# Kernel tuning notes

Hardware: AMD Instinct MI355X
Metric: run time of the kernel (lower is better)

Reference implementation:

```python
import jax, jax.numpy as jnp
import numpy as np

N_NODES = 50000
N_EDGES = 200000
HID = 32
EDGE_DIM = 16
EDGE_HIDDEN = 128


def setup_inputs() -> dict:
    key = jax.random.key(0)
    ks = jax.random.split(key, 10)
    nf = jax.random.normal(ks[0], (N_NODES, HID), dtype=jnp.float32)
    ef = jax.random.normal(ks[1], (N_EDGES, EDGE_DIM), dtype=jnp.float32)
    edge_src = jax.random.randint(ks[2], (N_EDGES,), 0, N_NODES, dtype=jnp.int32)
    edge_dst = jax.random.randint(ks[3], (N_EDGES,), 0, N_NODES, dtype=jnp.int32)
    # edge_func MLP: EDGE_DIM -> EDGE_HIDDEN -> HID*HID (per-edge weight matrix)
    s1 = 1.0 / np.sqrt(EDGE_DIM)
    s2 = 1.0 / np.sqrt(EDGE_HIDDEN)
    W1 = jax.random.uniform(ks[4], (EDGE_DIM, EDGE_HIDDEN), jnp.float32, -s1, s1)
    b1 = jax.random.uniform(ks[5], (EDGE_HIDDEN,), jnp.float32, -s1, s1)
    W2 = jax.random.uniform(ks[6], (EDGE_HIDDEN, HID * HID), jnp.float32, -s2, s2)
    b2 = jax.random.uniform(ks[7], (HID * HID,), jnp.float32, -s2, s2)
    bias = jnp.zeros((HID,), dtype=jnp.float32)  # NNConv output bias
    return {"nf": nf, "ef": ef, "edge_src": edge_src, "edge_dst": edge_dst,
            "W1": W1, "b1": b1, "W2": W2, "b2": b2, "bias": bias}


def reference(nf, ef, edge_src, edge_dst, W1, b1, W2, b2, bias):
    # edge network: per-edge weight matrix [E, HID, HID]
    h = jax.nn.relu(ef @ W1 + b1)
    We = (h @ W2 + b2).reshape(-1, HID, HID)
    # gather source features, per-edge matvec message [E, HID]
    msg = jnp.einsum('ei,eio->eo', nf[edge_src], We)
    # sum-aggregate messages at destination nodes, add bias
    agg = jax.ops.segment_sum(msg, edge_dst, num_segments=nf.shape[0])
    return agg + bias
```

## Files before the change

kernel.cpp:

```cpp
#include <hip/hip_runtime.h>


#define E_TOTAL   200000
#define N_NODES   50000
#define TILES     3125
#define OUT4      400000
#define OUT4_BLKS 1563
#define W2C_BLKS  64
#define NBLK      256
#define NTL_BIG   53
#define LDS_BYTES 163840

typedef short short8  __attribute__((ext_vector_type(8)));
typedef float f32x4   __attribute__((ext_vector_type(4)));
typedef float f32x16  __attribute__((ext_vector_type(16)));

__device__ __forceinline__ short f2bf(float f) {
    union { float f; unsigned u; } cv; cv.f = f;
    unsigned r = cv.u + 0x7fffu + ((cv.u >> 16) & 1u);
    return (short)(r >> 16);
}

__device__ __forceinline__ void gll16(const short* gsrc, short* ldst) {
    __builtin_amdgcn_global_load_lds(
        (const __attribute__((address_space(1))) unsigned int*)gsrc,
        (__attribute__((address_space(3))) unsigned int*)ldst, 16, 0, 0);
}

__global__ __launch_bounds__(256) void setup_kernel(const float* __restrict__ W2,
                                                    const float* __restrict__ bias,
                                                    float* __restrict__ out,
                                                    short* __restrict__ W2p) {
    int bid = blockIdx.x, tid = threadIdx.x;
    if (bid < OUT4_BLKS) {
        int i4 = bid * 256 + tid;
        if (i4 < OUT4) {
            float4 bv = *(const float4*)(bias + ((i4 & 7) << 2));
            *(float4*)(out + (size_t)i4 * 4) = bv;
        }
    } else {
        int q = (bid - OUT4_BLKS) * 256 + tid;
        int p  = q >> 13;
        int ch = q & 8191;
        int ks = ch >> 10, ct = (ch >> 6) & 15, lhg = (ch >> 5) & 1, cc = ch & 31;
        int c  = ct * 32 + cc;
        int i  = c >> 4, o15 = c & 15;
        int ci = i * 32 + p * 16 + o15;
        int kb = ks * 16 + lhg * 8;
        short8 pk;
        #pragma unroll
        for (int j = 0; j < 8; ++j) pk[j] = f2bf(W2[(size_t)(kb + j) * 1024 + ci]);
        *(short8*)(W2p + (size_t)q * 8) = pk;
    }
}

__global__ __launch_bounds__(512, 2) void mpnn_kernel(const float* __restrict__ nf,
                                                      const float* __restrict__ ef,
                                                      const int*   __restrict__ esrc,
                                                      const int*   __restrict__ edst,
                                                      const float* __restrict__ W1,
                                                      const float* __restrict__ b1,
                                                      const float* __restrict__ b2,
                                                      const short* __restrict__ W2p,
                                                      float* __restrict__ out) {
    extern __shared__ __align__(16) unsigned char smem[];
    short* W2s  = (short*)(smem);
    short* W1Ts = (short*)(smem + 131072);
    short* Hs   = (short*)(smem + 135168);
    float* XsT  = (float*)(smem + 151552);
    float* pbuf = (float*)(smem + 131072);

    const int tid = threadIdx.x;
    const int w   = tid >> 6;
    const int l31 = tid & 31;
    const int lh  = (tid >> 5) & 1;
    const int o15 = l31 & 15;
    const int ib  = l31 >> 4;
    const int xbw = lh ^ ib;
    const int bid = blockIdx.x;
    const int ntl = (bid < NTL_BIG) ? 13 : 12;
    const int itn = 2 * ntl;

    float4 xreg; short8 efreg;
    float  b2v0, b2v1;
    {
        #pragma unroll
        for (int j = 0; j < 16; ++j)
            gll16(W2p + w * 8192 + j * 512 + (tid & 63) * 8, W2s + w * 8192 + j * 512);
    }
    {
        int g = tid * 4; int i = g >> 7; int c0 = g & 127;
        float4 v = *(const float4*)(W1 + g);
        float vv[4] = {v.x, v.y, v.z, v.w};
        #pragma unroll
        for (int u = 0; u < 4; ++u) {
            int c = c0 + u;
            W1Ts[c * 16 + (((i >> 3) ^ ((c >> 2) & 1)) << 3) + (i & 7)] = f2bf(vv[u]);
        }
    }
    {
        int s = esrc[bid * 64 + (tid >> 3)];
        xreg = *(const float4*)(nf + (size_t)s * 32 + (tid & 7) * 4);
        int eL = l31 + ((w & 1) << 5);
        const float* ep = ef + (size_t)(bid * 64 + eL) * 16 + lh * 8;
        float4 a0 = *(const float4*)(ep);
        float4 a1 = *(const float4*)(ep + 4);
        efreg[0] = f2bf(a0.x); efreg[1] = f2bf(a0.y); efreg[2] = f2bf(a0.z); efreg[3] = f2bf(a0.w);
        efreg[4] = f2bf(a1.x); efreg[5] = f2bf(a1.y); efreg[6] = f2bf(a1.z); efreg[7] = f2bf(a1.w);
    }
    b2v0 = b2[(4 * w + ib) * 32 + o15];
    b2v1 = b2[(4 * w + 2 + ib) * 32 + o15];
    const int   cW1  = ((w >> 1) << 5) + l31;
    const float b1v  = b1[cW1];

    __syncthreads();
    const short8 w1frag = *(const short8*)(W1Ts + cW1 * 16 + ((lh ^ ((cW1 >> 2) & 1)) << 3));

    float  pv0 = 0.f, pv1 = 0.f;
    float *pa0 = out, *pa1 = out;

    for (int it = 0; it < itn; ++it) {
        const int pass = (it >= ntl) ? 1 : 0;
        const int tile = bid + (it - pass * ntl) * NBLK;
        const int ebase = tile * 64;

        if (it == ntl) {
            #pragma unroll
            for (int j = 0; j < 16; ++j)
                gll16(W2p + 65536 + w * 8192 + j * 512 + (tid & 63) * 8, W2s + w * 8192 + j * 512);
            b2v0 = b2[(4 * w + ib) * 32 + 16 + o15];
            b2v1 = b2[(4 * w + 2 + ib) * 32 + 16 + o15];
        }
        __syncthreads();

        {
            int e = tid >> 3, i4 = (tid & 7) * 4;
            XsT[(i4 + 0) * 68 + e] = xreg.x;
            XsT[(i4 + 1) * 68 + e] = xreg.y;
            XsT[(i4 + 2) * 68 + e] = xreg.z;
            XsT[(i4 + 3) * 68 + e] = xreg.w;
        }

        {
            f32x16 hacc;
            #pragma unroll
            for (int q = 0; q < 16; ++q) hacc[q] = 0.f;
            hacc = __builtin_amdgcn_mfma_f32_32x32x16_bf16(efreg, w1frag, hacc, 0, 0, 0);
            const int mh = w & 1, G1 = cW1 >> 3, j1 = cW1 & 7;
            #pragma unroll
            for (int r = 0; r < 16; ++r) {
                int ee = (r & 3) + ((r >> 2) << 3) + (lh << 2) + (mh << 5);
                float v = fmaxf(hacc[r] + b1v, 0.f);
                Hs[G1 * 512 + ((ee ^ (G1 & 7)) << 3) + j1] = f2bf(v);
            }
        }
        __syncthreads();

        int nit = it + 1; if (nit >= itn) nit = it;
        const int npass = (nit >= ntl) ? 1 : 0;
        const int nebase = (bid + (nit - npass * ntl) * NBLK) * 64;

        f32x16 acc00, acc01, acc10, acc11;
        #pragma unroll
        for (int q = 0; q < 16; ++q) { acc00[q] = 0.f; acc01[q] = 0.f; acc10[q] = 0.f; acc11[q] = 0.f; }
        int pre_s = 0;
        #pragma unroll
        for (int ks = 0; ks < 8; ++ks) {
            const int G  = 2 * ks + lh;
            const int ax = ((l31 ^ (G & 7)) << 3);
            short8 afr0 = *(const short8*)(Hs + G * 512 + ax);
            short8 afr1 = *(const short8*)(Hs + G * 512 + ax + 256);
            short8 bfr0 = *(const short8*)(W2s + ks * 8192 + (2 * w    ) * 512 + lh * 256 + l31 * 8);
            short8 bfr1 = *(const short8*)(W2s + ks * 8192 + (2 * w + 1) * 512 + lh * 256 + l31 * 8);
            acc00 = __builtin_amdgcn_mfma_f32_32x32x16_bf16(afr0, bfr0, acc00, 0, 0, 0);
            acc01 = __builtin_amdgcn_mfma_f32_32x32x16_bf16(afr1, bfr0, acc01, 0, 0, 0);
            acc10 = __builtin_amdgcn_mfma_f32_32x32x16_bf16(afr0, bfr1, acc10, 0, 0, 0);
            acc11 = __builtin_amdgcn_mfma_f32_32x32x16_bf16(afr1, bfr1, acc11, 0, 0, 0);
            if (ks == 1) pre_s = esrc[nebase + (tid >> 3)];
            if (ks == 2 && it > 0) {
                atomicAdd(pa0, pv0);
                atomicAdd(pa1, pv1);
            }
            if (ks == 3) {
                int eL = l31 + ((w & 1) << 5);
                const float* ep = ef + (size_t)(nebase + eL) * 16 + lh * 8;
                float4 a0 = *(const float4*)(ep);
                float4 a1 = *(const float4*)(ep + 4);
                efreg[0] = f2bf(a0.x); efreg[1] = f2bf(a0.y); efreg[2] = f2bf(a0.z); efreg[3] = f2bf(a0.w);
                efreg[4] = f2bf(a1.x); efreg[5] = f2bf(a1.y); efreg[6] = f2bf(a1.z); efreg[7] = f2bf(a1.w);
            }
            if (ks == 5) xreg = *(const float4*)(nf + (size_t)pre_s * 32 + (tid & 7) * 4);
        }

        const int xc0 = 4 * w + ib, xc1 = 4 * w + 2 + ib;
        float sv0[16], sv1[16];
        #pragma unroll
        for (int rq = 0; rq < 4; ++rq) {
            const int eb = 8 * rq + 4 * lh;
            f32x4 A0 = *(const f32x4*)(XsT + xc0 * 68 + eb);
            f32x4 B0 = *(const f32x4*)(XsT + xc1 * 68 + eb);
            f32x4 A1 = *(const f32x4*)(XsT + xc0 * 68 + eb + 32);
            f32x4 B1 = *(const f32x4*)(XsT + xc1 * 68 + eb + 32);
            #pragma unroll
            for (int u = 0; u < 4; ++u) {
                int r = rq * 4 + u;
                float v = A0[u] * (acc00[r] + b2v0) + B0[u] * (acc10[r] + b2v1);
                v += __shfl_xor(v, 16);
                sv0[r] = v;
                float v1 = A1[u] * (acc01[r] + b2v0) + B1[u] * (acc11[r] + b2v1);
                v1 += __shfl_xor(v1, 16);
                sv1[r] = v1;
            }
        }

        __syncthreads();
        #pragma unroll
        for (int r = 0; r < 16; ++r) {
            int e = (r & 3) + ((r >> 2) << 3) + (lh << 2) + (ib << 5);
            pbuf[(w << 10) + ((e ^ xbw) << 4) + o15] = ib ? sv1[r] : sv0[r];
        }
        __syncthreads();
        {
            int idx = tid;
            int e = idx >> 4, oo = idx & 15;
            int xbE = ((e >> 2) ^ (e >> 5)) & 1;
            int a = ((e ^ xbE) << 4) + oo;
            pv0 = ((pbuf[a]          + pbuf[a + 1024]) + (pbuf[a + 2048] + pbuf[a + 3072]))
                + ((pbuf[a + 4096]   + pbuf[a + 5120]) + (pbuf[a + 6144] + pbuf[a + 7168]));
            pa0 = out + (size_t)edst[ebase + e] * 32 + (pass << 4) + oo;
            idx = tid + 512;
            e = idx >> 4; oo = idx & 15;
            xbE = ((e >> 2) ^ (e >> 5)) & 1;
            a = ((e ^ xbE) << 4) + oo;
            pv1 = ((pbuf[a]          + pbuf[a + 1024]) + (pbuf[a + 2048] + pbuf[a + 3072]))
                + ((pbuf[a + 4096]   + pbuf[a + 5120]) + (pbuf[a + 6144] + pbuf[a + 7168]));
            pa1 = out + (size_t)edst[ebase + e] * 32 + (pass << 4) + oo;
        }
    }
    atomicAdd(pa0, pv0);
    atomicAdd(pa1, pv1);
}

extern "C" void kernel_launch(void* const* d_in, const int* in_sizes, int n_in,
                              void* d_out, int out_size, void* d_ws, size_t ws_size,
                              hipStream_t stream) {
    const float* nf   = (const float*)d_in[0];
    const float* ef   = (const float*)d_in[1];
    const int*   src  = (const int*)  d_in[2];
    const int*   dst  = (const int*)  d_in[3];
    const float* W1   = (const float*)d_in[4];
    const float* b1   = (const float*)d_in[5];
    const float* W2   = (const float*)d_in[6];
    const float* b2   = (const float*)d_in[7];
    const float* bias = (const float*)d_in[8];
    float* out = (float*)d_out;
    short* W2p = (short*)d_ws;

    static bool init_done = false;
    if (!init_done) {
        hipFuncSetAttribute((const void*)mpnn_kernel,
                            hipFuncAttributeMaxDynamicSharedMemorySize, LDS_BYTES);
        init_done = true;
    }

    setup_kernel<<<OUT4_BLKS + W2C_BLKS, 256, 0, stream>>>(W2, bias, out, W2p);
    mpnn_kernel<<<NBLK, 512, LDS_BYTES, stream>>>(nf, ef, src, dst, W1, b1, b2, W2p, out);
}
```

Baseline: 167.5 us.

## Stream W2 fragments from global into registers to double block count

```diff
diff --git a/kernel.cpp b/kernel.cpp
--- a/kernel.cpp
+++ b/kernel.cpp
@@ -7,9 +7,9 @@
 #define OUT4      400000
 #define OUT4_BLKS 1563
 #define W2C_BLKS  64
-#define NBLK      256
+#define NBLK      512
 #define NTL_BIG   53
-#define LDS_BYTES 163840
+#define LDS_BYTES 61952
 
 typedef short short8  __attribute__((ext_vector_type(8)));
 typedef float f32x4   __attribute__((ext_vector_type(4)));
@@ -19,12 +19,6 @@
     union { float f; unsigned u; } cv; cv.f = f;
     unsigned r = cv.u + 0x7fffu + ((cv.u >> 16) & 1u);
     return (short)(r >> 16);
-}
-
-__device__ __forceinline__ void gll16(const short* gsrc, short* ldst) {
-    __builtin_amdgcn_global_load_lds(
-        (const __attribute__((address_space(1))) unsigned int*)gsrc,
-        (__attribute__((address_space(3))) unsigned int*)ldst, 16, 0, 0);
 }
 
 __global__ __launch_bounds__(256) void setup_kernel(const float* __restrict__ W2,
@@ -54,7 +48,7 @@
     }
 }
 
-__global__ __launch_bounds__(512, 2) void mpnn_kernel(const float* __restrict__ nf,
+__global__ __launch_bounds__(512, 4) void mpnn_kernel(const float* __restrict__ nf,
                                                       const float* __restrict__ ef,
                                                       const int*   __restrict__ esrc,
                                                       const int*   __restrict__ edst,
@@ -64,11 +58,10 @@
                                                       const short* __restrict__ W2p,
                                                       float* __restrict__ out) {
     extern __shared__ __align__(16) unsigned char smem[];
-    short* W2s  = (short*)(smem);
-    short* W1Ts = (short*)(smem + 131072);
-    short* Hs   = (short*)(smem + 135168);
-    float* XsT  = (float*)(smem + 151552);
-    float* pbuf = (float*)(smem + 131072);
+    short* W1Ts = (short*)(smem);
+    short* Hs   = (short*)(smem + 4096);
+    float* XsT  = (float*)(smem + 20480);
+    float* pbuf = (float*)(smem + 29184);
 
     const int tid = threadIdx.x;
     const int w   = tid >> 6;
@@ -78,16 +71,12 @@
     const int ib  = l31 >> 4;
     const int xbw = lh ^ ib;
     const int bid = blockIdx.x;
-    const int ntl = (bid < NTL_BIG) ? 13 : 12;
+    const int ntl = (bid < NTL_BIG) ? 7 : 6;
     const int itn = 2 * ntl;
+    const int bofs = (w << 10) + lh * 256 + l31 * 8;
 
     float4 xreg; short8 efreg;
     float  b2v0, b2v1;
-    {
-        #pragma unroll
-        for (int j = 0; j < 16; ++j)
-            gll16(W2p + w * 8192 + j * 512 + (tid & 63) * 8, W2s + w * 8192 + j * 512);
-    }
     {
         int g = tid * 4; int i = g >> 7; int c0 = g & 127;
         float4 v = *(const float4*)(W1 + g);
@@ -117,7 +106,7 @@
     const short8 w1frag = *(const short8*)(W1Ts + cW1 * 16 + ((lh ^ ((cW1 >> 2) & 1)) << 3));
 
     float  pv0 = 0.f, pv1 = 0.f;
-    float *pa0 = out, *pa1 = out;
+    int    po0 = 0,   po1 = 0;
 
     for (int it = 0; it < itn; ++it) {
         const int pass = (it >= ntl) ? 1 : 0;
@@ -125,12 +114,15 @@
         const int ebase = tile * 64;
 
         if (it == ntl) {
-            #pragma unroll
-            for (int j = 0; j < 16; ++j)
-                gll16(W2p + 65536 + w * 8192 + j * 512 + (tid & 63) * 8, W2s + w * 8192 + j * 512);
             b2v0 = b2[(4 * w + ib) * 32 + 16 + o15];
             b2v1 = b2[(4 * w + 2 + ib) * 32 + 16 + o15];
         }
+
+        const short* Wb = W2p + (pass << 16) + bofs;
+        short8 bf[16];
+        bf[0] = *(const short8*)(Wb);           bf[1] = *(const short8*)(Wb + 512);
+        bf[2] = *(const short8*)(Wb + 8192);    bf[3] = *(const short8*)(Wb + 8704);
+
         __syncthreads();
 
         {
@@ -170,17 +162,15 @@
             const int ax = ((l31 ^ (G & 7)) << 3);
             short8 afr0 = *(const short8*)(Hs + G * 512 + ax);
             short8 afr1 = *(const short8*)(Hs + G * 512 + ax + 256);
-            short8 bfr0 = *(const short8*)(W2s + ks * 8192 + (2 * w    ) * 512 + lh * 256 + l31 * 8);
-            short8 bfr1 = *(const short8*)(W2s + ks * 8192 + (2 * w + 1) * 512 + lh * 256 + l31 * 8);
-            acc00 = __builtin_amdgcn_mfma_f32_32x32x16_bf16(afr0, bfr0, acc00, 0, 0, 0);
-            acc01 = __builtin_amdgcn_mfma_f32_32x32x16_bf16(afr1, bfr0, acc01, 0, 0, 0);
-            acc10 = __builtin_amdgcn_mfma_f32_32x32x16_bf16(afr0, bfr1, acc10, 0, 0, 0);
-            acc11 = __builtin_amdgcn_mfma_f32_32x32x16_bf16(afr1, bfr1, acc11, 0, 0, 0);
+            if (ks < 6) {
+                bf[2 * ks + 4] = *(const short8*)(Wb + (ks + 2) * 8192);
+                bf[2 * ks + 5] = *(const short8*)(Wb + (ks + 2) * 8192 + 512);
+            }
+            acc00 = __builtin_amdgcn_mfma_f32_32x32x16_bf16(afr0, bf[2 * ks    ], acc00, 0, 0, 0);
+            acc01 = __builtin_amdgcn_mfma_f32_32x32x16_bf16(afr1, bf[2 * ks    ], acc01, 0, 0, 0);
+            acc10 = __builtin_amdgcn_mfma_f32_32x32x16_bf16(afr0, bf[2 * ks + 1], acc10, 0, 0, 0);
+            acc11 = __builtin_amdgcn_mfma_f32_32x32x16_bf16(afr1, bf[2 * ks + 1], acc11, 0, 0, 0);
             if (ks == 1) pre_s = esrc[nebase + (tid >> 3)];
-            if (ks == 2 && it > 0) {
-                atomicAdd(pa0, pv0);
-                atomicAdd(pa1, pv1);
-            }
             if (ks == 3) {
                 int eL = l31 + ((w & 1) << 5);
                 const float* ep = ef + (size_t)(nebase + eL) * 16 + lh * 8;
@@ -190,10 +180,14 @@
                 efreg[4] = f2bf(a1.x); efreg[5] = f2bf(a1.y); efreg[6] = f2bf(a1.z); efreg[7] = f2bf(a1.w);
             }
             if (ks == 5) xreg = *(const float4*)(nf + (size_t)pre_s * 32 + (tid & 7) * 4);
+            if (ks == 6 && it > 0) {
+                atomicAdd(out + po0, pv0);
+                atomicAdd(out + po1, pv1);
+            }
         }
 
         const int xc0 = 4 * w + ib, xc1 = 4 * w + 2 + ib;
-        float sv0[16], sv1[16];
+        float* pslab = pbuf + (w << 10);
         #pragma unroll
         for (int rq = 0; rq < 4; ++rq) {
             const int eb = 8 * rq + 4 * lh;
@@ -206,18 +200,11 @@
                 int r = rq * 4 + u;
                 float v = A0[u] * (acc00[r] + b2v0) + B0[u] * (acc10[r] + b2v1);
                 v += __shfl_xor(v, 16);
-                sv0[r] = v;
                 float v1 = A1[u] * (acc01[r] + b2v0) + B1[u] * (acc11[r] + b2v1);
                 v1 += __shfl_xor(v1, 16);
-                sv1[r] = v1;
-            }
-        }
-
-        __syncthreads();
-        #pragma unroll
-        for (int r = 0; r < 16; ++r) {
-            int e = (r & 3) + ((r >> 2) << 3) + (lh << 2) + (ib << 5);
-            pbuf[(w << 10) + ((e ^ xbw) << 4) + o15] = ib ? sv1[r] : sv0[r];
+                int e = u + 8 * rq + 4 * lh + (ib << 5);
+                pslab[((e ^ xbw) << 4) + o15] = ib ? v1 : v;
+            }
         }
         __syncthreads();
         {
@@ -227,18 +214,18 @@
             int a = ((e ^ xbE) << 4) + oo;
             pv0 = ((pbuf[a]          + pbuf[a + 1024]) + (pbuf[a + 2048] + pbuf[a + 3072]))
                 + ((pbuf[a + 4096]   + pbuf[a + 5120]) + (pbuf[a + 6144] + pbuf[a + 7168]));
-            pa0 = out + (size_t)edst[ebase + e] * 32 + (pass << 4) + oo;
+            po0 = edst[ebase + e] * 32 + (pass << 4) + oo;
             idx = tid + 512;
             e = idx >> 4; oo = idx & 15;
             xbE = ((e >> 2) ^ (e >> 5)) & 1;
             a = ((e ^ xbE) << 4) + oo;
             pv1 = ((pbuf[a]          + pbuf[a + 1024]) + (pbuf[a + 2048] + pbuf[a + 3072]))
                 + ((pbuf[a + 4096]   + pbuf[a + 5120]) + (pbuf[a + 6144] + pbuf[a + 7168]));
-            pa1 = out + (size_t)edst[ebase + e] * 32 + (pass << 4) + oo;
-        }
-    }
-    atomicAdd(pa0, pv0);
-    atomicAdd(pa1, pv1);
+            po1 = edst[ebase + e] * 32 + (pass << 4) + oo;
+        }
+    }
+    atomicAdd(out + po0, pv0);
+    atomicAdd(out + po1, pv1);
 }
 
 extern "C" void kernel_launch(void* const* d_in, const int* in_sizes, int n_in,
@@ -256,13 +243,6 @@
     float* out = (float*)d_out;
     short* W2p = (short*)d_ws;
 
-    static bool init_done = false;
-    if (!init_done) {
-        hipFuncSetAttribute((const void*)mpnn_kernel,
-                            hipFuncAttributeMaxDynamicSharedMemorySize, LDS_BYTES);
-        init_done = true;
-    }
-
     setup_kernel<<<OUT4_BLKS + W2C_BLKS, 256, 0, stream>>>(W2, bias, out, W2p);
     mpnn_kernel<<<NBLK, 512, LDS_BYTES, stream>>>(nf, ef, src, dst, W1, b1, b2, W2p, out);
 }
```

After: 268.5 us. +60.3%, slower.
